# Kernel tuning notes

Measured on AMD Instinct MI355X. Metric: run time of the kernel, lower is better.

## Reference

```python
import jax, jax.numpy as jnp
import numpy as np

B, T, C = 4, 2048, 2048
H, N = 32, 64          # n_head, head_size; H*N == C (n_dim_att == n_dim)
DMIX, DDEC = 32, 64    # hardcoded LoRA dims in module


def setup_inputs() -> dict:
    key = jax.random.key(0)
    ks = jax.random.split(key, 24)
    u = lambda k, s, lo, hi: jax.random.uniform(k, s, jnp.float32, lo, hi)
    g = lambda k, s: jax.random.normal(k, s, jnp.float32) * 0.02
    return {
        'x': jax.random.normal(ks[0], (B, T, C), jnp.float32),
        'shift_state_in': jax.random.normal(ks[1], (B, C), jnp.float32),
        'wkv_state_in': jnp.zeros((B, H, N, N), jnp.float32),
        'time_maa_x': u(ks[2], (C,), 0.0, 1.0),
        'time_maa_r': u(ks[3], (C,), 0.0, 1.0),
        'time_maa_k': u(ks[4], (C,), 0.0, 1.0),
        'time_maa_v': u(ks[5], (C,), 0.0, 1.0),
        'time_maa_w': u(ks[6], (C,), 0.0, 1.0),
        'time_maa_v2': u(ks[7], (C,), 0.0, 1.0),
        'time_maa_w1': u(ks[8], (C, DMIX * 5), -0.01, 0.01),
        'time_maa_w2': u(ks[9], (5, DMIX, C), -0.01, 0.01),
        'time_decay': u(ks[10], (C,), -6.0, -1.0),
        'time_decay_w1': u(ks[11], (C, DDEC), -0.01, 0.01),
        'time_decay_w2': u(ks[12], (DDEC, C), -0.01, 0.01),
        'time_value2_w1': u(ks[13], (C, DDEC), -0.01, 0.01),
        'time_value2_w2': u(ks[14], (DDEC, C), -0.01, 0.01),
        'W_r': g(ks[15], (C, C)),
        'W_k': g(ks[16], (C, C)),
        'W_v': g(ks[17], (C, C)),
        'W_o': g(ks[18], (C, C)),
        'ln_w': jnp.ones((C,), jnp.float32),
        'ln_b': jnp.zeros((C,), jnp.float32),
    }


def _to_heads(a):
    # [B,T,C] -> [T,B,H,N] for time-major scan
    return a.reshape(B, T, H, N).transpose(1, 0, 2, 3)


def reference(x, shift_state_in, wkv_state_in,
              time_maa_x, time_maa_r, time_maa_k, time_maa_v, time_maa_w, time_maa_v2,
              time_maa_w1, time_maa_w2,
              time_decay, time_decay_w1, time_decay_w2,
              time_value2_w1, time_value2_w2,
              W_r, W_k, W_v, W_o, ln_w, ln_b):
    # token shift
    dxprev = jnp.concatenate([shift_state_in[:, None, :], x[:, :-1]], axis=1) - x
    xxx = x + dxprev * time_maa_x
    hmix = jnp.tanh(xxx @ time_maa_w1).reshape(B, T, 5, DMIX)
    mix = jnp.einsum('btfd,fdc->fbtc', hmix, time_maa_w2)  # [5,B,T,C]
    mr, mk, mv, mw, mv2 = mix
    xr = x + dxprev * (time_maa_r + mr)
    xk = x + dxprev * (time_maa_k + mk)
    xv = x + dxprev * (time_maa_v + mv)
    xw = x + dxprev * (time_maa_w + mw)
    xv2 = x + dxprev * (time_maa_v2 + mv2)

    r = xr @ W_r
    k = xk @ W_k
    v = xv @ W_v
    v2 = xv2 @ W_v + jnp.tanh(xv2 @ time_value2_w1) @ time_value2_w2
    w = time_decay + jnp.tanh(xw @ time_decay_w1) @ time_decay_w2
    decay = jnp.exp(-jnp.exp(w))         # per-channel, data-dependent
    k = k * (1.0 - decay)

    rh, kh, vh, dh = _to_heads(r), _to_heads(k), _to_heads(v), _to_heads(decay)

    def step(state, inputs):
        # state: [B,H,N,N] (k-dim x v-dim); u (time_faaaa) is zero in this variant
        r_t, k_t, v_t, d_t = inputs  # each [B,H,N]
        y = jnp.einsum('bhi,bhij->bhj', r_t, state)
        state = state * d_t[..., None] + k_t[..., None] * v_t[..., None, :]
        return state, y

    wkv_state_out, ys = jax.lax.scan(step, wkv_state_in, (rh, kh, vh, dh))
    y = ys.transpose(1, 0, 2, 3).reshape(B, T, C)
    y = y + v2
    # LayerNorm over n_dim_att
    mu = jnp.mean(y, axis=-1, keepdims=True)
    var = jnp.var(y, axis=-1, keepdims=True)
    y = (y - mu) / jnp.sqrt(var + 1e-5) * ln_w + ln_b
    y = y @ W_o
    return y, x[:, -1], wkv_state_out
```

## Files before the change

### kernel.cpp

```cpp
#include <hip/hip_runtime.h>
#include <hip/hip_bf16.h>
#include <cstdio>


typedef __attribute__((ext_vector_type(8))) short bf16x8;
typedef __attribute__((ext_vector_type(4))) float floatx4;

#define T_DIM 2048
#define C_DIM 2048
#define B_DIM 4
#define M_ROWS (B_DIM * T_DIM)

typedef const unsigned int __attribute__((address_space(1)))* gas1_t;
typedef unsigned int __attribute__((address_space(3)))* las3_t;
__device__ __forceinline__ void gl_lds16(const void* g, void* l) {
    __builtin_amdgcn_global_load_lds((gas1_t)g, (las3_t)l, 16, 0, 0);
}

__global__ __launch_bounds__(256) void k_transpose(
    const float* __restrict__ in, void* __restrict__ out,
    int R, int Cin, int to_bf16)
{
    __shared__ float tile[32][33];
    const int tx = threadIdx.x & 31, ty = threadIdx.x >> 5;
    const int cbase = blockIdx.x * 32, rbase = blockIdx.y * 32;
#pragma unroll
    for (int i = 0; i < 4; i++) {
        int r = rbase + ty + i * 8;
        int c = cbase + tx;
        tile[ty + i * 8][tx] = (c < Cin) ? in[(size_t)r * Cin + c] : 0.0f;
    }
    __syncthreads();
    if (to_bf16) {
        __hip_bfloat16* ob = (__hip_bfloat16*)out;
#pragma unroll
        for (int i = 0; i < 4; i++) {
            int c = cbase + ty + i * 8;
            ob[(size_t)c * R + rbase + tx] = __float2bfloat16(tile[tx][ty + i * 8]);
        }
    } else {
        float* of = (float*)out;
#pragma unroll
        for (int i = 0; i < 4; i++) {
            int c = cbase + ty + i * 8;
            of[(size_t)c * R + rbase + tx] = tile[tx][ty + i * 8];
        }
    }
}

__global__ __launch_bounds__(256) void k_xx(
    const float* __restrict__ x, const float* __restrict__ shift,
    const float* __restrict__ tmx,
    __hip_bfloat16* __restrict__ XX, float* __restrict__ xlast)
{
    const int row = blockIdx.x;
    const int b = row >> 11, t = row & 2047;
    const int c0 = threadIdx.x * 8;
    const float* xrow = x + (size_t)row * C_DIM;
    const float* prow = (t == 0) ? (shift + (size_t)b * C_DIM) : (xrow - C_DIM);
    float4 xa = ((const float4*)(xrow + c0))[0];
    float4 xb = ((const float4*)(xrow + c0))[1];
    float4 pa = ((const float4*)(prow + c0))[0];
    float4 pb = ((const float4*)(prow + c0))[1];
    float xv8[8] = {xa.x, xa.y, xa.z, xa.w, xb.x, xb.y, xb.z, xb.w};
    float pv8[8] = {pa.x, pa.y, pa.z, pa.w, pb.x, pb.y, pb.z, pb.w};
    union { bf16x8 v8; __hip_bfloat16 e[8]; } u;
#pragma unroll
    for (int j = 0; j < 8; j++)
        u.e[j] = __float2bfloat16(fmaf(pv8[j] - xv8[j], tmx[c0 + j], xv8[j]));
    *(bf16x8*)(XX + (size_t)row * C_DIM + c0) = u.v8;
    if (t == T_DIM - 1) {
        ((float4*)(xlast + (size_t)b * C_DIM + c0))[0] = xa;
        ((float4*)(xlast + (size_t)b * C_DIM + c0))[1] = xb;
    }
}

__global__ __launch_bounds__(256) void k_gemm_h(
    const __hip_bfloat16* __restrict__ A,
    const __hip_bfloat16* __restrict__ Bt,
    float* __restrict__ Hout)
{
    __shared__ __hip_bfloat16 As[64 * 32];
    __shared__ __hip_bfloat16 Bs[256 * 32];
    const int tid = threadIdx.x;
    const int m0 = blockIdx.x * 64;
    const int wave = tid >> 6, lane = tid & 63;
    const int fcol = lane & 15, quad = lane >> 4;
    floatx4 acc[16];
#pragma unroll
    for (int i = 0; i < 16; i++) acc[i] = (floatx4){0.f, 0.f, 0.f, 0.f};

    const int rA = tid >> 2, kcA = (tid & 3) * 8;
    const __hip_bfloat16* gA = A + (size_t)(m0 + rA) * 2048 + kcA;
    __hip_bfloat16* lA = As + tid * 8;
    const __hip_bfloat16* gB[4];
    __hip_bfloat16* lB[4];
#pragma unroll
    for (int s = 0; s < 4; s++) {
        int q = tid + 256 * s;
        gB[s] = Bt + (size_t)(q >> 2) * 2048 + (q & 3) * 8;
        lB[s] = Bs + q * 8;
    }
    for (int kk = 0; kk < 2048; kk += 32) {
        gl_lds16(gA + kk, lA);
#pragma unroll
        for (int s = 0; s < 4; s++) gl_lds16(gB[s] + kk, lB[s]);
        __syncthreads();
        bf16x8 aF = *(const bf16x8*)(As + (wave * 16 + fcol) * 32 + quad * 8);
#pragma unroll
        for (int ni = 0; ni < 16; ni++) {
            bf16x8 bF = *(const bf16x8*)(Bs + (ni * 16 + fcol) * 32 + quad * 8);
            acc[ni] = __builtin_amdgcn_mfma_f32_16x16x32_bf16(aF, bF, acc[ni], 0, 0, 0);
        }
        __syncthreads();
    }
#pragma unroll
    for (int ni = 0; ni < 16; ni++) {
        int col = ni * 16 + fcol;
#pragma unroll
        for (int g = 0; g < 4; g++) {
            int row = m0 + wave * 16 + quad * 4 + g;
            Hout[(size_t)row * 256 + col] = tanhf(acc[ni][g]);
        }
    }
}

__global__ __launch_bounds__(256) void k_gemm_n64(
    const __hip_bfloat16* __restrict__ A,
    const __hip_bfloat16* __restrict__ Bt,
    __hip_bfloat16* __restrict__ G)
{
    __shared__ __hip_bfloat16 As[64 * 32];
    __shared__ __hip_bfloat16 Bs[64 * 32];
    const int tid = threadIdx.x;
    const int m0 = blockIdx.x * 64;
    const int wave = tid >> 6, lane = tid & 63;
    const int fcol = lane & 15, quad = lane >> 4;
    floatx4 acc[4];
#pragma unroll
    for (int i = 0; i < 4; i++) acc[i] = (floatx4){0.f, 0.f, 0.f, 0.f};

    const int r = tid >> 2, kc = (tid & 3) * 8;
    const __hip_bfloat16* gA = A + (size_t)(m0 + r) * 2048 + kc;
    const __hip_bfloat16* gB = Bt + (size_t)r * 2048 + kc;
    __hip_bfloat16* lA = As + tid * 8;
    __hip_bfloat16* lB = Bs + tid * 8;
    for (int kk = 0; kk < 2048; kk += 32) {
        gl_lds16(gA + kk, lA);
        gl_lds16(gB + kk, lB);
        __syncthreads();
        bf16x8 aF = *(const bf16x8*)(As + (wave * 16 + fcol) * 32 + quad * 8);
#pragma unroll
        for (int ni = 0; ni < 4; ni++) {
            bf16x8 bF = *(const bf16x8*)(Bs + (ni * 16 + fcol) * 32 + quad * 8);
            acc[ni] = __builtin_amdgcn_mfma_f32_16x16x32_bf16(aF, bF, acc[ni], 0, 0, 0);
        }
        __syncthreads();
    }
#pragma unroll
    for (int ni = 0; ni < 4; ni++) {
        int col = ni * 16 + fcol;
#pragma unroll
        for (int g = 0; g < 4; g++) {
            int row = m0 + wave * 16 + quad * 4 + g;
            G[(size_t)row * 64 + col] = __float2bfloat16(tanhf(acc[ni][g]));
        }
    }
}

__global__ __launch_bounds__(256) void k_mixapply(
    const float* __restrict__ x, const float* __restrict__ shift,
    const float* __restrict__ H, const float* __restrict__ w2,
    const float* __restrict__ tmr, const float* __restrict__ tmk,
    const float* __restrict__ tmv, const float* __restrict__ tmw,
    const float* __restrict__ tmv2,
    __hip_bfloat16* __restrict__ xr, __hip_bfloat16* __restrict__ xk,
    __hip_bfloat16* __restrict__ xv, __hip_bfloat16* __restrict__ xw,
    __hip_bfloat16* __restrict__ xv2)
{
    __shared__ float hsm[16][160];
    const int row0 = blockIdx.x * 16;
    const int b = row0 >> 11;
    const int tid = threadIdx.x;
    for (int idx = tid; idx < 16 * 160; idx += 256)
        hsm[idx / 160][idx % 160] = H[(size_t)(row0 + idx / 160) * 256 + idx % 160];
    __syncthreads();
    const int c0 = tid * 8;
    const float* maas[5] = {tmr, tmk, tmv, tmw, tmv2};
    __hip_bfloat16* outs[5] = {xr, xk, xv, xw, xv2};
    for (int rc = 0; rc < 16; rc += 8) {
#pragma unroll
        for (int f = 0; f < 5; f++) {
            float acc[8][8];
#pragma unroll
            for (int r = 0; r < 8; r++)
#pragma unroll
                for (int j = 0; j < 8; j++) acc[r][j] = 0.f;
#pragma unroll 4
            for (int d = 0; d < 32; d++) {
                const float4* wp = (const float4*)(w2 + (size_t)(f * 32 + d) * 2048 + c0);
                float4 p0 = wp[0], p1 = wp[1];
                float wv[8] = {p0.x, p0.y, p0.z, p0.w, p1.x, p1.y, p1.z, p1.w};
#pragma unroll
                for (int r = 0; r < 8; r++) {
                    float h = hsm[rc + r][f * 32 + d];
#pragma unroll
                    for (int j = 0; j < 8; j++) acc[r][j] = fmaf(h, wv[j], acc[r][j]);
                }
            }
            const float* maa = maas[f];
            float m8[8];
#pragma unroll
            for (int j = 0; j < 8; j++) m8[j] = maa[c0 + j];
#pragma unroll
            for (int r = 0; r < 8; r++) {
                int row = row0 + rc + r;
                int t = row & 2047;
                const float* xrow = x + (size_t)row * C_DIM;
                const float* prow = (t == 0) ? (shift + (size_t)b * C_DIM) : (xrow - C_DIM);
                float4 xa = ((const float4*)(xrow + c0))[0];
                float4 xb = ((const float4*)(xrow + c0))[1];
                float4 pa = ((const float4*)(prow + c0))[0];
                float4 pb = ((const float4*)(prow + c0))[1];
                float xv8[8] = {xa.x, xa.y, xa.z, xa.w, xb.x, xb.y, xb.z, xb.w};
                float pv8[8] = {pa.x, pa.y, pa.z, pa.w, pb.x, pb.y, pb.z, pb.w};
                union { bf16x8 v8; __hip_bfloat16 e[8]; } u;
#pragma unroll
                for (int j = 0; j < 8; j++) {
                    float dx = pv8[j] - xv8[j];
                    u.e[j] = __float2bfloat16(fmaf(dx, m8[j] + acc[r][j], xv8[j]));
                }
                *(bf16x8*)(outs[f] + (size_t)row * C_DIM + c0) = u.v8;
            }
        }
    }
}

__global__ __launch_bounds__(512, 2) void k_gemm256(
    const __hip_bfloat16* __restrict__ A,
    const __hip_bfloat16* __restrict__ Bt,
    int mode,
    float* __restrict__ outF, __hip_bfloat16* __restrict__ outB)
{
    constexpr int K = 2048;
    constexpr int NT = K / 32;
    __shared__ __hip_bfloat16 LA[4][256 * 32];
    __shared__ __hip_bfloat16 LB[4][256 * 32];
    const int tid = threadIdx.x;
    const int bid = blockIdx.x;
    const int n0 = (bid & 7) * 256;
    const int m0 = (bid >> 3) * 256;
    const int wave = tid >> 6, lane = tid & 63;
    const int wm = (wave >> 2) * 128, wn = (wave & 3) * 64;
    const int fcol = lane & 15, quad = lane >> 4;

    floatx4 acc[8][4];
#pragma unroll
    for (int mi = 0; mi < 8; mi++)
#pragma unroll
        for (int ni = 0; ni < 4; ni++)
            acc[mi][ni] = (floatx4){0.f, 0.f, 0.f, 0.f};

    const int ch0 = wave * 2, ch1 = wave * 2 + 1;
    const int rr = lane >> 2, kc = (lane & 3) * 8;
    const __hip_bfloat16* pA0 = A  + (size_t)(m0 + ch0 * 16 + rr) * K + kc;
    const __hip_bfloat16* pA1 = A  + (size_t)(m0 + ch1 * 16 + rr) * K + kc;
    const __hip_bfloat16* pB0 = Bt + (size_t)(n0 + ch0 * 16 + rr) * K + kc;
    const __hip_bfloat16* pB1 = Bt + (size_t)(n0 + ch1 * 16 + rr) * K + kc;
    const int lo0 = ch0 * 512 + lane * 8;
    const int lo1 = ch1 * 512 + lane * 8;

    int ns = 0;
    for (; ns < 3; ++ns) {
        gl_lds16(pA0 + ns * 32, &LA[ns][lo0]);
        gl_lds16(pA1 + ns * 32, &LA[ns][lo1]);
        gl_lds16(pB0 + ns * 32, &LB[ns][lo0]);
        gl_lds16(pB1 + ns * 32, &LB[ns][lo1]);
    }
    for (int t = 0; t < NT; ++t) {
        if (t < NT - 2)       asm volatile("s_waitcnt vmcnt(8)" ::: "memory");
        else if (t == NT - 2) asm volatile("s_waitcnt vmcnt(4)" ::: "memory");
        else                  asm volatile("s_waitcnt vmcnt(0)" ::: "memory");
        asm volatile("s_barrier" ::: "memory");
        if (ns < NT) {
            const int sl = ns & 3;
            gl_lds16(pA0 + ns * 32, &LA[sl][lo0]);
            gl_lds16(pA1 + ns * 32, &LA[sl][lo1]);
            gl_lds16(pB0 + ns * 32, &LB[sl][lo0]);
            gl_lds16(pB1 + ns * 32, &LB[sl][lo1]);
            ++ns;
        }
        const int st = t & 3;
        const __hip_bfloat16* ab = &LA[st][(wm + fcol) * 32 + quad * 8];
        const __hip_bfloat16* bb = &LB[st][(wn + fcol) * 32 + quad * 8];
        bf16x8 bF[4];
#pragma unroll
        for (int ni = 0; ni < 4; ni++)
            bF[ni] = *(const bf16x8*)(bb + ni * 512);
#pragma unroll
        for (int mi = 0; mi < 8; mi++) {
            bf16x8 aF = *(const bf16x8*)(ab + mi * 512);
#pragma unroll
            for (int ni = 0; ni < 4; ni++)
                acc[mi][ni] = __builtin_amdgcn_mfma_f32_16x16x32_bf16(
                    aF, bF[ni], acc[mi][ni], 0, 0, 0);
        }
    }
#pragma unroll
    for (int mi = 0; mi < 8; mi++) {
#pragma unroll
        for (int ni = 0; ni < 4; ni++) {
            int rbase = m0 + wm + mi * 16 + quad * 4;
            int ccol = n0 + wn + ni * 16 + fcol;
#pragma unroll
            for (int g = 0; g < 4; g++) {
                size_t idx = (size_t)(rbase + g) * 2048 + ccol;
                float val = acc[mi][ni][g];
                if (mode == 0) outF[idx] = val;
                else           outB[idx] = __float2bfloat16(val);
            }
        }
    }
}

__global__ __launch_bounds__(256) void k_gemm64(
    const __hip_bfloat16* __restrict__ A0, const __hip_bfloat16* __restrict__ B0,
    const __hip_bfloat16* __restrict__ A1, const __hip_bfloat16* __restrict__ B1,
    float* __restrict__ decayOut, const float* __restrict__ tdec,
    __hip_bfloat16* __restrict__ v2Out)
{
    constexpr int K = 64;
    __shared__ __hip_bfloat16 As[128 * 32];
    __shared__ __hip_bfloat16 Bs[128 * 32];
    const int tid = threadIdx.x;
    const int op = blockIdx.x >> 10;
    const int id = blockIdx.x & 1023;
    const int xcd = id & 7, jj = id >> 3;
    const int m0 = (((xcd << 3) | (jj & 7))) * 128;
    const int n0 = (jj >> 3) * 128;
    const __hip_bfloat16* A = op ? A1 : A0;
    const __hip_bfloat16* Bt = op ? B1 : B0;
    const int wave = tid >> 6, lane = tid & 63;
    const int wm = (wave >> 1) * 64, wn = (wave & 1) * 64;
    const int fcol = lane & 15, quad = lane >> 4;

    floatx4 acc[4][4];
#pragma unroll
    for (int mi = 0; mi < 4; mi++)
#pragma unroll
        for (int ni = 0; ni < 4; ni++)
            acc[mi][ni] = (floatx4){0.f, 0.f, 0.f, 0.f};

    const int q0 = tid, q1 = tid + 256;
    const int r0 = q0 >> 2, kc0 = (q0 & 3) * 8;
    const int r1 = q1 >> 2, kc1 = (q1 & 3) * 8;
    const __hip_bfloat16* gA0 = A + (size_t)(m0 + r0) * K + kc0;
    const __hip_bfloat16* gA1 = A + (size_t)(m0 + r1) * K + kc1;
    const __hip_bfloat16* gB0 = Bt + (size_t)(n0 + r0) * K + kc0;
    const __hip_bfloat16* gB1 = Bt + (size_t)(n0 + r1) * K + kc1;
    __hip_bfloat16* lA0 = As + q0 * 8; __hip_bfloat16* lA1 = As + q1 * 8;
    __hip_bfloat16* lB0 = Bs + q0 * 8; __hip_bfloat16* lB1 = Bs + q1 * 8;

    for (int kk = 0; kk < K; kk += 32) {
        gl_lds16(gA0 + kk, lA0);
        gl_lds16(gA1 + kk, lA1);
        gl_lds16(gB0 + kk, lB0);
        gl_lds16(gB1 + kk, lB1);
        __syncthreads();
        bf16x8 aF[4], bF[4];
#pragma unroll
        for (int mi = 0; mi < 4; mi++)
            aF[mi] = *(const bf16x8*)(As + (wm + mi * 16 + fcol) * 32 + quad * 8);
#pragma unroll
        for (int ni = 0; ni < 4; ni++)
            bF[ni] = *(const bf16x8*)(Bs + (wn + ni * 16 + fcol) * 32 + quad * 8);
#pragma unroll
        for (int mi = 0; mi < 4; mi++)
#pragma unroll
            for (int ni = 0; ni < 4; ni++)
                acc[mi][ni] = __builtin_amdgcn_mfma_f32_16x16x32_bf16(
                    aF[mi], bF[ni], acc[mi][ni], 0, 0, 0);
        __syncthreads();
    }
#pragma unroll
    for (int mi = 0; mi < 4; mi++) {
#pragma unroll
        for (int ni = 0; ni < 4; ni++) {
            int rbase = m0 + wm + mi * 16 + quad * 4;
            int ccol = n0 + wn + ni * 16 + fcol;
#pragma unroll
            for (int g = 0; g < 4; g++) {
                size_t idx = (size_t)(rbase + g) * 2048 + ccol;
                float val = acc[mi][ni][g];
                if (op == 0) {
                    decayOut[idx] = expf(-expf(val + tdec[ccol]));
                } else {
                    v2Out[idx] = __float2bfloat16(__bfloat162float(v2Out[idx]) + val);
                }
            }
        }
    }
}

__global__ __launch_bounds__(256) void k_scan_chunked(
    const __hip_bfloat16* __restrict__ r, const __hip_bfloat16* __restrict__ k,
    const __hip_bfloat16* __restrict__ v, const float* __restrict__ dec,
    const float* __restrict__ state_in,
    __hip_bfloat16* __restrict__ y, float* __restrict__ state_out)
{
    __shared__ __hip_bfloat16 Rs[2][64 * 64];
    __shared__ __hip_bfloat16 Ks[2][64 * 64];
    __shared__ __hip_bfloat16 Vs[2][64 * 64];
    __shared__ float          Dsb[2][64 * 64];
    __shared__ __hip_bfloat16 Ys[2][64 * 64];
    __shared__ __hip_bfloat16 Am[64 * 72];
    __shared__ __hip_bfloat16 Bm[64 * 72];
    __shared__ __hip_bfloat16 VT[64 * 72];
    __shared__ __hip_bfloat16 CT[64 * 72];
    __shared__ __hip_bfloat16 ST[64 * 72];
    __shared__ __hip_bfloat16 Pm[64 * 72];
    __shared__ float part[4][64];
    __shared__ float efin[64];

    const int tid = threadIdx.x;
    const int bh = blockIdx.x, b = bh >> 5, h = bh & 31;
    const int wave = tid >> 6, lane = tid & 63;
    const int fcol = lane & 15, quad = lane >> 4;
    const int ci = tid & 63, seg = tid >> 6;

    floatx4 sfr[4];
    {
        const float* sp = state_in + (size_t)bh * 4096;
#pragma unroll
        for (int n = 0; n < 4; n++)
#pragma unroll
            for (int g = 0; g < 4; g++)
                sfr[n][g] = sp[(size_t)(16 * wave + quad * 4 + g) * 64 + 16 * n + fcol];
    }

    const size_t cbase0 = (size_t)b * T_DIM * C_DIM + (size_t)h * 64;

    auto stage = [&](int cc, int buf) {
        const size_t cb = cbase0 + (size_t)cc * 64 * C_DIM;
        const int q0 = tid, q1 = tid + 256;
        const size_t o0 = (size_t)(q0 >> 3) * C_DIM + (q0 & 7) * 8;
        const size_t o1 = (size_t)(q1 >> 3) * C_DIM + (q1 & 7) * 8;
        gl_lds16(r + cb + o0, &Rs[buf][q0 * 8]);
        gl_lds16(r + cb + o1, &Rs[buf][q1 * 8]);
        gl_lds16(k + cb + o0, &Ks[buf][q0 * 8]);
        gl_lds16(k + cb + o1, &Ks[buf][q1 * 8]);
        gl_lds16(v + cb + o0, &Vs[buf][q0 * 8]);
        gl_lds16(v + cb + o1, &Vs[buf][q1 * 8]);
        gl_lds16(y + cb + o0, &Ys[buf][q0 * 8]);
        gl_lds16(y + cb + o1, &Ys[buf][q1 * 8]);
#pragma unroll
        for (int s = 0; s < 4; s++) {
            int q = tid + 256 * s;
            gl_lds16(dec + cb + (size_t)(q >> 4) * C_DIM + (q & 15) * 4,
                     &Dsb[buf][q * 4]);
        }
    };

    stage(0, 0);

    for (int c = 0; c < 32; c++) {
        const int cur = c & 1, nxt = cur ^ 1;
        const size_t cb = cbase0 + (size_t)c * 64 * C_DIM;

        if (c == 0) asm volatile("s_waitcnt vmcnt(0)" ::: "memory");
        else        asm volatile("s_waitcnt vmcnt(16)" ::: "memory");
        asm volatile("s_waitcnt lgkmcnt(0)" ::: "memory");
        __builtin_amdgcn_s_barrier();
        __builtin_amdgcn_sched_barrier(0);

        if (c + 1 < 32) stage(c + 1, nxt);

        {
#pragma unroll
            for (int n = 0; n < 4; n++)
#pragma unroll
                for (int g = 0; g < 4; g++)
                    ST[(size_t)(16 * n + fcol) * 72 + 16 * wave + quad * 4 + g] =
                        __float2bfloat16(sfr[n][g]);
            float p = 1.0f;
#pragma unroll
            for (int u = 0; u < 16; u++) p *= Dsb[cur][(seg * 16 + u) * 64 + ci];
            part[seg][ci] = p;
        }
        asm volatile("s_waitcnt lgkmcnt(0)" ::: "memory");
        __builtin_amdgcn_s_barrier();
        __builtin_amdgcn_sched_barrier(0);

        {
            float p0 = part[0][ci], p1 = part[1][ci], p2 = part[2][ci], p3 = part[3][ci];
            float pre = 1.0f;
            if (seg > 0) pre *= p0;
            if (seg > 1) pre *= p1;
            if (seg > 2) pre *= p2;
            float tot = p0 * p1 * p2 * p3;
            if (seg == 0) efin[ci] = tot;
            float e = pre;
#pragma unroll
            for (int u = 0; u < 16; u++) {
                int t = seg * 16 + u;
                float d = Dsb[cur][t * 64 + ci];
                float rv = __bfloat162float(Rs[cur][t * 64 + ci]);
                float kv = __bfloat162float(Ks[cur][t * 64 + ci]) * (1.0f - d);
                Am[t * 72 + ci] = __float2bfloat16(rv * e);
                e *= d;
                float bb = kv * __builtin_amdgcn_rcpf(e);
                Bm[t * 72 + ci] = __float2bfloat16(bb);
                CT[ci * 72 + t] = __float2bfloat16(bb * tot);
            }
#pragma unroll
            for (int u = 0; u < 16; u++) {
                int t = seg * 16 + ((u + (ci & 15)) & 15);
                VT[ci * 72 + t] = Vs[cur][t * 64 + ci];
            }
        }
        asm volatile("s_waitcnt lgkmcnt(0)" ::: "memory");
        __builtin_amdgcn_s_barrier();
        __builtin_amdgcn_sched_barrier(0);

        {
            bf16x8 af[2];
#pragma unroll
            for (int kk = 0; kk < 2; kk++)
                af[kk] = *(const bf16x8*)(Am + (16 * wave + fcol) * 72 + kk * 32 + quad * 8);
            floatx4 pfr[4], yfr[4];
#pragma unroll
            for (int n = 0; n < 4; n++) {
                pfr[n] = (floatx4){0.f, 0.f, 0.f, 0.f};
                yfr[n] = (floatx4){0.f, 0.f, 0.f, 0.f};
#pragma unroll
                for (int kk = 0; kk < 2; kk++) {
                    bf16x8 bF = *(const bf16x8*)(Bm + (16 * n + fcol) * 72 + kk * 32 + quad * 8);
                    bf16x8 sF = *(const bf16x8*)(ST + (16 * n + fcol) * 72 + kk * 32 + quad * 8);
                    pfr[n] = __builtin_amdgcn_mfma_f32_16x16x32_bf16(af[kk], bF, pfr[n], 0, 0, 0);
                    yfr[n] = __builtin_amdgcn_mfma_f32_16x16x32_bf16(af[kk], sF, yfr[n], 0, 0, 0);
                }
            }
#pragma unroll
            for (int n = 0; n < 4; n++)
#pragma unroll
                for (int g = 0; g < 4; g++) {
                    int t = 16 * wave + quad * 4 + g;
                    int s = 16 * n + fcol;
                    Pm[t * 72 + s] = (s < t) ? __float2bfloat16(pfr[n][g])
                                             : __float2bfloat16(0.0f);
                }
            float eg[4];
#pragma unroll
            for (int g = 0; g < 4; g++) eg[g] = efin[16 * wave + quad * 4 + g];
#pragma unroll
            for (int n = 0; n < 4; n++)
#pragma unroll
                for (int g = 0; g < 4; g++) sfr[n][g] *= eg[g];
            bf16x8 pf[2], cf[2];
#pragma unroll
            for (int kk = 0; kk < 2; kk++) {
                pf[kk] = *(const bf16x8*)(Pm + (16 * wave + fcol) * 72 + kk * 32 + quad * 8);
                cf[kk] = *(const bf16x8*)(CT + (16 * wave + fcol) * 72 + kk * 32 + quad * 8);
            }
#pragma unroll
            for (int n = 0; n < 4; n++) {
#pragma unroll
                for (int kk = 0; kk < 2; kk++) {
                    bf16x8 vF = *(const bf16x8*)(VT + (16 * n + fcol) * 72 + kk * 32 + quad * 8);
                    yfr[n] = __builtin_amdgcn_mfma_f32_16x16x32_bf16(pf[kk], vF, yfr[n], 0, 0, 0);
                    sfr[n] = __builtin_amdgcn_mfma_f32_16x16x32_bf16(cf[kk], vF, sfr[n], 0, 0, 0);
                }
            }
#pragma unroll
            for (int n = 0; n < 4; n++)
#pragma unroll
                for (int g = 0; g < 4; g++) {
                    int t = 16 * wave + quad * 4 + g;
                    int s = 16 * n + fcol;
                    size_t addr = cb + (size_t)t * C_DIM + s;
                    float yv = __bfloat162float(Ys[cur][t * 64 + s]) + yfr[n][g];
                    y[addr] = __float2bfloat16(yv);
                }
        }
    }
    {
        float* so = state_out + (size_t)bh * 4096;
#pragma unroll
        for (int n = 0; n < 4; n++)
#pragma unroll
            for (int g = 0; g < 4; g++)
                so[(size_t)(16 * wave + quad * 4 + g) * 64 + 16 * n + fcol] = sfr[n][g];
    }
}

__global__ __launch_bounds__(256) void k_addln(
    __hip_bfloat16* __restrict__ y,
    const float* __restrict__ lnw, const float* __restrict__ lnb)
{
    __shared__ float ls[4], ls2[4];
    const int row = blockIdx.x;
    const size_t base = (size_t)row * C_DIM;
    const int tid = threadIdx.x;
    const int c0 = tid * 8;
    union { bf16x8 v8; __hip_bfloat16 e[8]; } uin;
    uin.v8 = *(const bf16x8*)(y + base + c0);
    float vbuf[8];
#pragma unroll
    for (int j = 0; j < 8; j++) vbuf[j] = __bfloat162float(uin.e[j]);
    float s = 0.f, s2 = 0.f;
#pragma unroll
    for (int j = 0; j < 8; j++) { s += vbuf[j]; s2 += vbuf[j] * vbuf[j]; }
#pragma unroll
    for (int off = 32; off > 0; off >>= 1) {
        s += __shfl_down(s, off, 64);
        s2 += __shfl_down(s2, off, 64);
    }
    const int w = tid >> 6;
    if ((tid & 63) == 0) { ls[w] = s; ls2[w] = s2; }
    __syncthreads();
    float S = ls[0] + ls[1] + ls[2] + ls[3];
    float S2 = ls2[0] + ls2[1] + ls2[2] + ls2[3];
    float mu = S * (1.0f / C_DIM);
    float var = S2 * (1.0f / C_DIM) - mu * mu;
    float rs = rsqrtf(var + 1e-5f);
    union { bf16x8 v8; __hip_bfloat16 e[8]; } u;
#pragma unroll
    for (int j = 0; j < 8; j++) {
        int ccc = c0 + j;
        u.e[j] = __float2bfloat16((vbuf[j] - mu) * rs * lnw[ccc] + lnb[ccc]);
    }
    *(bf16x8*)(y + base + c0) = u.v8;
}

extern "C" void kernel_launch(void* const* d_in, const int* in_sizes, int n_in,
                              void* d_out, int out_size, void* d_ws, size_t ws_size,
                              hipStream_t stream)
{
    const float* x     = (const float*)d_in[0];
    const float* shift = (const float*)d_in[1];
    const float* wkvin = (const float*)d_in[2];
    const float* tmx   = (const float*)d_in[3];
    const float* tmr   = (const float*)d_in[4];
    const float* tmk   = (const float*)d_in[5];
    const float* tmv   = (const float*)d_in[6];
    const float* tmw   = (const float*)d_in[7];
    const float* tmv2  = (const float*)d_in[8];
    const float* w1    = (const float*)d_in[9];
    const float* w2    = (const float*)d_in[10];
    const float* tdec  = (const float*)d_in[11];
    const float* dw1   = (const float*)d_in[12];
    const float* dw2   = (const float*)d_in[13];
    const float* vw1   = (const float*)d_in[14];
    const float* vw2   = (const float*)d_in[15];
    const float* Wr    = (const float*)d_in[16];
    const float* Wk    = (const float*)d_in[17];
    const float* Wv    = (const float*)d_in[18];
    const float* Wo    = (const float*)d_in[19];
    const float* lnw   = (const float*)d_in[20];
    const float* lnb   = (const float*)d_in[21];

    const size_t SZ_XBF = (size_t)M_ROWS * C_DIM * 2;
    const size_t SZ_WBF = (size_t)C_DIM * C_DIM * 2;
    char* ws = (char*)d_ws;
    size_t off = 0;
    __hip_bfloat16* S0 = (__hip_bfloat16*)(ws + off); off += SZ_XBF;
    __hip_bfloat16* S1 = (__hip_bfloat16*)(ws + off); off += SZ_XBF;
    __hip_bfloat16* S2 = (__hip_bfloat16*)(ws + off); off += SZ_XBF;
    __hip_bfloat16* S3 = (__hip_bfloat16*)(ws + off); off += SZ_XBF;
    __hip_bfloat16* S4 = (__hip_bfloat16*)(ws + off); off += SZ_XBF;
    char* D = ws + off; off += (size_t)M_ROWS * C_DIM * 4;
    __hip_bfloat16* XX    = (__hip_bfloat16*)D;
    float*          Hbuf  = (float*)(D + SZ_XBF);
    float*          decay = (float*)D;
    __hip_bfloat16* WrT = (__hip_bfloat16*)(ws + off); off += SZ_WBF;
    __hip_bfloat16* WkT = (__hip_bfloat16*)(ws + off); off += SZ_WBF;
    __hip_bfloat16* WvT = (__hip_bfloat16*)(ws + off); off += SZ_WBF;
    __hip_bfloat16* WoT = (__hip_bfloat16*)(ws + off); off += SZ_WBF;
    __hip_bfloat16* w1tb  = (__hip_bfloat16*)(ws + off); off += (size_t)256 * 2048 * 2;
    __hip_bfloat16* dw1t  = (__hip_bfloat16*)(ws + off); off += (size_t)64 * 2048 * 2;
    __hip_bfloat16* vw1t  = (__hip_bfloat16*)(ws + off); off += (size_t)64 * 2048 * 2;
    __hip_bfloat16* dw2t  = (__hip_bfloat16*)(ws + off); off += (size_t)2048 * 64 * 2;
    __hip_bfloat16* vw2t  = (__hip_bfloat16*)(ws + off); off += (size_t)2048 * 64 * 2;
    __hip_bfloat16* Gd    = (__hip_bfloat16*)(ws + off); off += (size_t)M_ROWS * 64 * 2;
    __hip_bfloat16* Gv    = (__hip_bfloat16*)(ws + off); off += (size_t)M_ROWS * 64 * 2;
    if (ws_size < off) {
        fprintf(stderr, "kernel_launch: ws too small (%zu < %zu)\n", ws_size, off);
        return;
    }

    float* out_y     = (float*)d_out;
    float* out_xlast = out_y + (size_t)M_ROWS * C_DIM;
    float* out_state = out_xlast + (size_t)B_DIM * C_DIM;

    k_transpose<<<dim3(8, 64),  256, 0, stream>>>(w1,  w1tb, 2048, 160, 1);
    k_transpose<<<dim3(2, 64),  256, 0, stream>>>(dw1, dw1t, 2048, 64, 1);
    k_transpose<<<dim3(2, 64),  256, 0, stream>>>(vw1, vw1t, 2048, 64, 1);
    k_transpose<<<dim3(64, 2),  256, 0, stream>>>(dw2, dw2t, 64, 2048, 1);
    k_transpose<<<dim3(64, 2),  256, 0, stream>>>(vw2, vw2t, 64, 2048, 1);
    k_transpose<<<dim3(64, 64), 256, 0, stream>>>(Wr, WrT, 2048, 2048, 1);
    k_transpose<<<dim3(64, 64), 256, 0, stream>>>(Wk, WkT, 2048, 2048, 1);
    k_transpose<<<dim3(64, 64), 256, 0, stream>>>(Wv, WvT, 2048, 2048, 1);
    k_transpose<<<dim3(64, 64), 256, 0, stream>>>(Wo, WoT, 2048, 2048, 1);

    k_xx<<<M_ROWS, 256, 0, stream>>>(x, shift, tmx, XX, out_xlast);
    k_gemm_h<<<128, 256, 0, stream>>>(XX, w1tb, Hbuf);
    k_mixapply<<<512, 256, 0, stream>>>(x, shift, Hbuf, w2,
                                        tmr, tmk, tmv, tmw, tmv2,
                                        S0, S1, S2, S3, S4);
    k_gemm_n64<<<128, 256, 0, stream>>>(S3, dw1t, Gd);
    k_gemm_n64<<<128, 256, 0, stream>>>(S4, vw1t, Gv);
    k_gemm256<<<256, 512, 0, stream>>>(S1, WkT, 1, nullptr, S3);
    k_gemm256<<<256, 512, 0, stream>>>(S0, WrT, 1, nullptr, S1);
    k_gemm256<<<256, 512, 0, stream>>>(S2, WvT, 1, nullptr, S0);
    k_gemm256<<<256, 512, 0, stream>>>(S4, WvT, 1, nullptr, S2);
    k_gemm64<<<2048, 256, 0, stream>>>(Gd, dw2t, Gv, vw2t, decay, tdec, S2);
    k_scan_chunked<<<128, 256, 0, stream>>>(S1, S3, S0, decay, wkvin, S2, out_state);
    k_addln<<<M_ROWS, 256, 0, stream>>>(S2, lnw, lnb);
    k_gemm256<<<256, 512, 0, stream>>>(S2, WoT, 0, out_y, nullptr);

    (void)in_sizes; (void)n_in; (void)out_size;
}
```

Before: 1.205 ms.

## Rewrite mix-apply LoRA projection as bf16 MFMA tiles with LDS-staged inputs

The k_mixapply kernel computed the five LoRA mix projections (H @ time_maa_w2) with scalar fp32 FMAs and re-read x rows from global memory. It is replaced by k_mixfused, which tiles 32 rows by 256 columns per block. The tile's x rows (plus the shifted previous row) and the bf16 H tile are staged in LDS via global_load_lds, and the per-factor mix is computed with bf16 MFMA against a newly transposed bf16 w2. k_gemm_h now writes H in bf16, halving that buffer's traffic, at the cost of extra rounding of H and of the mix terms before the final interpolation.

After: 1.137 ms. 1.06x faster.

```diff
diff --git a/kernel.cpp b/kernel.cpp
--- a/kernel.cpp
+++ b/kernel.cpp
@@ -78,7 +78,7 @@
 __global__ __launch_bounds__(256) void k_gemm_h(
     const __hip_bfloat16* __restrict__ A,
     const __hip_bfloat16* __restrict__ Bt,
-    float* __restrict__ Hout)
+    __hip_bfloat16* __restrict__ Hout)
 {
     __shared__ __hip_bfloat16 As[64 * 32];
     __shared__ __hip_bfloat16 Bs[256 * 32];
@@ -120,7 +120,7 @@
 #pragma unroll
         for (int g = 0; g < 4; g++) {
             int row = m0 + wave * 16 + quad * 4 + g;
-            Hout[(size_t)row * 256 + col] = tanhf(acc[ni][g]);
+            Hout[(size_t)row * 256 + col] = __float2bfloat16(tanhf(acc[ni][g]));
         }
     }
 }
@@ -168,9 +168,10 @@
     }
 }
 
-__global__ __launch_bounds__(256) void k_mixapply(
+__global__ __launch_bounds__(256) void k_mixfused(
     const float* __restrict__ x, const float* __restrict__ shift,
-    const float* __restrict__ H, const float* __restrict__ w2,
+    const __hip_bfloat16* __restrict__ Hb,
+    const __hip_bfloat16* __restrict__ w2T,
     const float* __restrict__ tmr, const float* __restrict__ tmk,
     const float* __restrict__ tmv, const float* __restrict__ tmw,
     const float* __restrict__ tmv2,
@@ -178,60 +179,96 @@
     __hip_bfloat16* __restrict__ xv, __hip_bfloat16* __restrict__ xw,
     __hip_bfloat16* __restrict__ xv2)
 {
-    __shared__ float hsm[16][160];
-    const int row0 = blockIdx.x * 16;
-    const int b = row0 >> 11;
+    __shared__ float          xp[33 * 256];
+    __shared__ __hip_bfloat16 Hs[32 * 256];
+    __shared__ __hip_bfloat16 mixS[32 * 256];
+
     const int tid = threadIdx.x;
-    for (int idx = tid; idx < 16 * 160; idx += 256)
-        hsm[idx / 160][idx % 160] = H[(size_t)(row0 + idx / 160) * 256 + idx % 160];
-    __syncthreads();
-    const int c0 = tid * 8;
+    const int bid = blockIdx.x;
+    const int n0 = (bid & 7) * 256;
+    const int m0 = (bid >> 3) * 32;
+    const int wave = tid >> 6, lane = tid & 63;
+    const int fcol = lane & 15, quad = lane >> 4;
+    const int wm = (wave >> 1) * 16, wn = (wave & 1) * 128;
+
+#pragma unroll
+    for (int i = 0; i < 8; i++) {
+        int row = i * 4 + wave;
+        gl_lds16(x + (size_t)(m0 + row) * C_DIM + n0 + lane * 4,
+                 xp + (row + 1) * 256 + lane * 4);
+    }
+    if (wave == 0) {
+        const float* src = (m0 & 2047)
+            ? (x + (size_t)(m0 - 1) * C_DIM + n0)
+            : (shift + (size_t)(m0 >> 11) * C_DIM + n0);
+        gl_lds16(src + lane * 4, xp + lane * 4);
+    }
+#pragma unroll
+    for (int i = 0; i < 4; i++) {
+        int q = tid + 256 * i;
+        gl_lds16(Hb + (size_t)(m0 + (q >> 5)) * 256 + (q & 31) * 8,
+                 Hs + (q >> 5) * 256 + (q & 31) * 8);
+    }
+    asm volatile("s_waitcnt vmcnt(0) lgkmcnt(0)" ::: "memory");
+    __builtin_amdgcn_s_barrier();
+    __builtin_amdgcn_sched_barrier(0);
+
     const float* maas[5] = {tmr, tmk, tmv, tmw, tmv2};
     __hip_bfloat16* outs[5] = {xr, xk, xv, xw, xv2};
-    for (int rc = 0; rc < 16; rc += 8) {
-#pragma unroll
-        for (int f = 0; f < 5; f++) {
-            float acc[8][8];
-#pragma unroll
-            for (int r = 0; r < 8; r++)
-#pragma unroll
-                for (int j = 0; j < 8; j++) acc[r][j] = 0.f;
-#pragma unroll 4
-            for (int d = 0; d < 32; d++) {
-                const float4* wp = (const float4*)(w2 + (size_t)(f * 32 + d) * 2048 + c0);
-                float4 p0 = wp[0], p1 = wp[1];
-                float wv[8] = {p0.x, p0.y, p0.z, p0.w, p1.x, p1.y, p1.z, p1.w};
-#pragma unroll
-                for (int r = 0; r < 8; r++) {
-                    float h = hsm[rc + r][f * 32 + d];
-#pragma unroll
-                    for (int j = 0; j < 8; j++) acc[r][j] = fmaf(h, wv[j], acc[r][j]);
-                }
-            }
-            const float* maa = maas[f];
-            float m8[8];
-#pragma unroll
-            for (int j = 0; j < 8; j++) m8[j] = maa[c0 + j];
-#pragma unroll
-            for (int r = 0; r < 8; r++) {
-                int row = row0 + rc + r;
-                int t = row & 2047;
-                const float* xrow = x + (size_t)row * C_DIM;
-                const float* prow = (t == 0) ? (shift + (size_t)b * C_DIM) : (xrow - C_DIM);
-                float4 xa = ((const float4*)(xrow + c0))[0];
-                float4 xb = ((const float4*)(xrow + c0))[1];
-                float4 pa = ((const float4*)(prow + c0))[0];
-                float4 pb = ((const float4*)(prow + c0))[1];
+    const int cc = tid & 31, c0 = cc * 8, rb = tid >> 5;
+
+#pragma unroll
+    for (int f = 0; f < 5; f++) {
+        {
+            bf16x8 aF = *(const bf16x8*)(Hs + (wm + fcol) * 256 + f * 32 + quad * 8);
+            floatx4 acc[8];
+#pragma unroll
+            for (int nf = 0; nf < 8; nf++) {
+                bf16x8 bF = *(const bf16x8*)(
+                    w2T + (size_t)(n0 + wn + nf * 16 + fcol) * 160 + f * 32 + quad * 8);
+                acc[nf] = __builtin_amdgcn_mfma_f32_16x16x32_bf16(
+                    aF, bF, (floatx4){0.f, 0.f, 0.f, 0.f}, 0, 0, 0);
+            }
+#pragma unroll
+            for (int nf = 0; nf < 8; nf++)
+#pragma unroll
+                for (int g = 0; g < 4; g++)
+                    mixS[(wm + quad * 4 + g) * 256 + wn + nf * 16 + fcol] =
+                        __float2bfloat16(acc[nf][g]);
+        }
+        asm volatile("s_waitcnt lgkmcnt(0)" ::: "memory");
+        __builtin_amdgcn_s_barrier();
+        __builtin_amdgcn_sched_barrier(0);
+
+        {
+            float4 ma = ((const float4*)(maas[f] + n0 + c0))[0];
+            float4 mb = ((const float4*)(maas[f] + n0 + c0))[1];
+            float m8[8] = {ma.x, ma.y, ma.z, ma.w, mb.x, mb.y, mb.z, mb.w};
+#pragma unroll
+            for (int i = 0; i < 4; i++) {
+                int row = rb + 8 * i;
+                float4 xa = ((const float4*)(xp + (row + 1) * 256 + c0))[0];
+                float4 xb = ((const float4*)(xp + (row + 1) * 256 + c0))[1];
+                float4 pa = ((const float4*)(xp + row * 256 + c0))[0];
+                float4 pb = ((const float4*)(xp + row * 256 + c0))[1];
                 float xv8[8] = {xa.x, xa.y, xa.z, xa.w, xb.x, xb.y, xb.z, xb.w};
                 float pv8[8] = {pa.x, pa.y, pa.z, pa.w, pb.x, pb.y, pb.z, pb.w};
+                union { bf16x8 v8; __hip_bfloat16 e[8]; } mu;
+                mu.v8 = *(const bf16x8*)(mixS + row * 256 + c0);
                 union { bf16x8 v8; __hip_bfloat16 e[8]; } u;
 #pragma unroll
                 for (int j = 0; j < 8; j++) {
                     float dx = pv8[j] - xv8[j];
-                    u.e[j] = __float2bfloat16(fmaf(dx, m8[j] + acc[r][j], xv8[j]));
+                    float mixv = __bfloat162float(mu.e[j]);
+                    u.e[j] = __float2bfloat16(fmaf(dx, m8[j] + mixv, xv8[j]));
                 }
-                *(bf16x8*)(outs[f] + (size_t)row * C_DIM + c0) = u.v8;
-            }
+                *(bf16x8*)(outs[f] + (size_t)(m0 + row) * C_DIM + n0 + c0) = u.v8;
+            }
+        }
+        if (f < 4) {
+            asm volatile("s_waitcnt lgkmcnt(0)" ::: "memory");
+            __builtin_amdgcn_s_barrier();
+            __builtin_amdgcn_sched_barrier(0);
         }
     }
 }
@@ -670,7 +707,7 @@
     __hip_bfloat16* S4 = (__hip_bfloat16*)(ws + off); off += SZ_XBF;
     char* D = ws + off; off += (size_t)M_ROWS * C_DIM * 4;
     __hip_bfloat16* XX    = (__hip_bfloat16*)D;
-    float*          Hbuf  = (float*)(D + SZ_XBF);
+    __hip_bfloat16* Hb    = (__hip_bfloat16*)(D + SZ_XBF);
     float*          decay = (float*)D;
     __hip_bfloat16* WrT = (__hip_bfloat16*)(ws + off); off += SZ_WBF;
     __hip_bfloat16* WkT = (__hip_bfloat16*)(ws + off); off += SZ_WBF;
@@ -683,6 +720,7 @@
     __hip_bfloat16* vw2t  = (__hip_bfloat16*)(ws + off); off += (size_t)2048 * 64 * 2;
     __hip_bfloat16* Gd    = (__hip_bfloat16*)(ws + off); off += (size_t)M_ROWS * 64 * 2;
     __hip_bfloat16* Gv    = (__hip_bfloat16*)(ws + off); off += (size_t)M_ROWS * 64 * 2;
+    __hip_bfloat16* w2T   = (__hip_bfloat16*)(ws + off); off += (size_t)2048 * 160 * 2;
     if (ws_size < off) {
         fprintf(stderr, "kernel_launch: ws too small (%zu < %zu)\n", ws_size, off);
         return;
@@ -697,16 +735,17 @@
     k_transpose<<<dim3(2, 64),  256, 0, stream>>>(vw1, vw1t, 2048, 64, 1);
     k_transpose<<<dim3(64, 2),  256, 0, stream>>>(dw2, dw2t, 64, 2048, 1);
     k_transpose<<<dim3(64, 2),  256, 0, stream>>>(vw2, vw2t, 64, 2048, 1);
+    k_transpose<<<dim3(64, 5),  256, 0, stream>>>(w2,  w2T,  160, 2048, 1);
     k_transpose<<<dim3(64, 64), 256, 0, stream>>>(Wr, WrT, 2048, 2048, 1);
     k_transpose<<<dim3(64, 64), 256, 0, stream>>>(Wk, WkT, 2048, 2048, 1);
     k_transpose<<<dim3(64, 64), 256, 0, stream>>>(Wv, WvT, 2048, 2048, 1);
     k_transpose<<<dim3(64, 64), 256, 0, stream>>>(Wo, WoT, 2048, 2048, 1);
 
     k_xx<<<M_ROWS, 256, 0, stream>>>(x, shift, tmx, XX, out_xlast);
-    k_gemm_h<<<128, 256, 0, stream>>>(XX, w1tb, Hbuf);
-    k_mixapply<<<512, 256, 0, stream>>>(x, shift, Hbuf, w2,
-                                        tmr, tmk, tmv, tmw, tmv2,
-                                        S0, S1, S2, S3, S4);
+    k_gemm_h<<<128, 256, 0, stream>>>(XX, w1tb, Hb);
+    k_mixfused<<<2048, 256, 0, stream>>>(x, shift, Hb, w2T,
+                                         tmr, tmk, tmv, tmw, tmv2,
+                                         S0, S1, S2, S3, S4);
     k_gemm_n64<<<128, 256, 0, stream>>>(S3, dw1t, Gd);
     k_gemm_n64<<<128, 256, 0, stream>>>(S4, vw1t, Gv);
     k_gemm256<<<256, 512, 0, stream>>>(S1, WkT, 1, nullptr, S3);
```
